# Kernel optimization log

Measured on AMD Instinct MI355X. Metric: run time of the kernel, lower is better.

Reference implementation:

```python
import jax, jax.numpy as jnp
import numpy as np
from jax import lax

EQN, GR = 10, 4
N, C, H, W = 8, 64, 16, 16


def _build_a(h, w):
    num = h * w
    a = np.zeros((num, EQN, 4 * num), np.float32)
    for i in range(num):
        right = (i + 1) % w != 0 and i + 1 < num
        down = i + w < num
        if right:
            a[i, 0, 2 * num + i] = 1.0; a[i, 0, i + 1] = -1.0
            a[i, 2, 2 * num + i] = 1.0; a[i, 2, 2 * num + i + 1] = -1.0
            a[i, 4, i] = 1.0;           a[i, 4, i + 1] = -1.0
            a[i, 6, 3 * num + i] = 1.0; a[i, 6, 3 * num + i + 1] = -1.0
            a[i, 8, num + i] = 1.0;     a[i, 8, num + i + 1] = -1.0
        if down:
            a[i, 1, 3 * num + i] = 1.0; a[i, 1, num + i + w] = -1.0
            a[i, 3, 3 * num + i] = 1.0; a[i, 3, 3 * num + i + w] = -1.0
            a[i, 5, num + i] = 1.0;     a[i, 5, num + i + w] = -1.0
            a[i, 7, 2 * num + i] = 1.0; a[i, 7, 2 * num + i + w] = -1.0
            a[i, 9, i] = 1.0;           a[i, 9, i + w] = -1.0
    last = num - 1
    a[last, 0, 2 * num + last] = 1.0
    a[last, 1, 3 * num + last] = 1.0
    a[last, 2, 2 * num + last] = 1.0
    a[last, 3, 3 * num + last] = 1.0
    a[last, 4, last] = 1.0
    a[last, 5, num + last] = 1.0
    a[last, 6, 3 * num + last] = 1.0
    a[last, 7, 2 * num + last] = 1.0
    a[last, 8, num + last] = 1.0
    a[last, 9, last] = 1.0
    return jnp.asarray(a)


def _conv(x, w, b):
    y = lax.conv_general_dilated(x, w, (1, 1), 'SAME',
                                 dimension_numbers=('NCHW', 'OIHW', 'NCHW'))
    return y + b[None, :, None, None]


def _lrelu(v):
    return jnp.where(v >= 0, v, 0.01 * v)


def setup_inputs() -> dict:
    key = jax.random.key(0)
    ks = jax.random.split(key, 18)
    s = 0.05
    d = {
        'x':   jax.random.normal(ks[0], (N, C, H, W), jnp.float32),
        'a':   _build_a(H, W),
        'gw1': jax.random.normal(ks[1], (C, C, 3, 3), jnp.float32) * s,
        'gb1': jnp.zeros((C,), jnp.float32),
        'gw2': jax.random.normal(ks[2], (EQN * GR, C, 3, 3), jnp.float32) * s,
        'gb2': jnp.zeros((EQN * GR,), jnp.float32),
        'aw1': jax.random.normal(ks[3], (C, C, 3, 3), jnp.float32) * s,
        'ab1': jnp.zeros((C,), jnp.float32),
        'aw2': jax.random.normal(ks[4], (EQN * GR, C, 3, 3), jnp.float32) * s,
        'ab2': jnp.zeros((EQN * GR,), jnp.float32),
        'sw1': jax.random.normal(ks[5], (C // 2, C, 1, 1), jnp.float32) * s,
        'sb1': jnp.zeros((C // 2,), jnp.float32),
        'sw2': jax.random.normal(ks[6], (4 * GR, C // 2, 1, 1), jnp.float32) * s,
        'sb2': jnp.zeros((4 * GR,), jnp.float32),
        'ins_w': jnp.ones((4 * GR,), jnp.float32),
        'ins_b': jnp.zeros((4 * GR,), jnp.float32),
        'pw':  jax.random.normal(ks[7], (128, 4 * GR, 3, 3), jnp.float32) * s,
        'pb':  jnp.zeros((128,), jnp.float32),
    }
    return d


def reference(x, a, gw1, gb1, gw2, gb2, aw1, ab1, aw2, ab2,
              sw1, sb1, sw2, sb2, ins_w, ins_b, pw, pb):
    n, c, h, w = x.shape
    num = h * w
    # attention / gradient / squeeze-excite branches
    att = jax.nn.sigmoid(_conv(_lrelu(_conv(x, aw1, ab1)), aw2, ab2))   # (n, eqn*gr, h, w)
    g   = _conv(_lrelu(_conv(x, gw1, gb1)), gw2, gb2)                   # (n, eqn*gr, h, w)
    pooled = x.mean(axis=(2, 3), keepdims=True)
    se = jax.nn.sigmoid(_conv(_lrelu(_conv(pooled, sw1, sb1)), sw2, sb2))  # (n, 4*gr, 1, 1)
    # reshape channels (gr, eqn), flatten batch*group, move pixel axis first
    att_r = att.reshape(n * GR, EQN, num).transpose(0, 2, 1)   # (ng, num, eqn)
    g_r   = g.reshape(n * GR, EQN, num).transpose(0, 2, 1)
    # weighted flow-equation system (done for all ng at once; the torch chunked
    # loop is only a memory optimization, math is identical)
    A = (a[None] * att_r[..., None]).reshape(n * GR, num * EQN, 4 * num)
    B = (g_r * att_r).reshape(n * GR, num * EQN)
    ATA = jnp.einsum('bki,bkj->bij', A, A)          # (ng, 4num, 4num)
    ATB = jnp.einsum('bki,bk->bi', A, B)            # (ng, 4num)
    ATA = ATA + jnp.eye(4 * num, dtype=x.dtype) * 1e-12
    sol = jnp.linalg.solve(ATA, ATB[..., None])     # (ng, 4num, 1)
    y = sol.reshape(n, 4 * GR, h, w)
    # GroupNorm(1, 4*gr): normalize over (C,H,W) per sample, per-channel affine
    mu = y.mean(axis=(1, 2, 3), keepdims=True)
    var = ((y - mu) ** 2).mean(axis=(1, 2, 3), keepdims=True)
    y = (y - mu) / jnp.sqrt(var + 1e-5)
    y = y * ins_w[None, :, None, None] + ins_b[None, :, None, None]
    y = se * y
    return _conv(y, pw, pb)
```

## Files before the change

### kernel.cpp

```cpp
#include <hip/hip_runtime.h>
#include <hip/hip_bf16.h>


#define NIT 64

__global__ __launch_bounds__(256) void k_se(
    const float* __restrict__ x, const float* __restrict__ sw1,
    const float* __restrict__ sb1, const float* __restrict__ sw2,
    const float* __restrict__ sb2, float* __restrict__ se)
{
  int n = blockIdx.x, t = threadIdx.x;
  __shared__ float part[64*4];
  __shared__ float pooled[64];
  __shared__ float h1[32];
  int c = t >> 2, q = t & 3;
  const float* xp = x + ((n*64 + c)*256) + q*64;
  float s = 0.f;
  #pragma unroll 8
  for (int j = 0; j < 64; ++j) s += xp[j];
  part[c*4+q] = s;
  __syncthreads();
  if (t < 64) pooled[t] = (part[t*4+0]+part[t*4+1]+part[t*4+2]+part[t*4+3]) * (1.f/256.f);
  __syncthreads();
  if (t < 32) {
    float a = sb1[t];
    for (int c2 = 0; c2 < 64; ++c2) a = fmaf(sw1[t*64+c2], pooled[c2], a);
    h1[t] = a >= 0.f ? a : 0.01f*a;
  }
  __syncthreads();
  if (t < 16) {
    float a = sb2[t];
    for (int c2 = 0; c2 < 32; ++c2) a = fmaf(sw2[t*32+c2], h1[c2], a);
    se[n*16+t] = 1.f/(1.f+__expf(-a));
  }
}

__device__ __forceinline__ float lane_bcast(float v, int src){
  return __int_as_float(__builtin_amdgcn_readlane(__float_as_int(v), src));
}

template<int CO_T, int CO_TOTAL, int ACT>
__global__ __launch_bounds__(1024) void k_convw(
    const float* __restrict__ xg, const float* __restrict__ xa,
    const float* __restrict__ wg, const float* __restrict__ bg,
    const float* __restrict__ wa, const float* __restrict__ ba,
    float* __restrict__ outg, float* __restrict__ outa)
{
  const int tiles = CO_TOTAL / CO_T;
  int b = blockIdx.x;
  int tile = b % tiles; int rem = b / tiles;
  int br = rem & 1;     int n = rem >> 1;
  const float* xin  = br ? xa : xg;
  const float* w    = br ? wa : wg;
  const float* bias = br ? ba : bg;
  float* outp       = br ? outa : outg;
  int co_base = tile * CO_T;
  int t = threadIdx.x;
  int pix = t & 255, qc = t >> 8;
  int pr = pix >> 4, pc = pix & 15;
  int lane = t & 63;
  int cib = qc*16;
  __shared__ float xs[64*324];
  __shared__ float part[3][CO_T][256];
  int cil = cib + (lane & 15);
  float wv[CO_T*9];
  #pragma unroll
  for (int co = 0; co < CO_T; ++co) {
    const float* wp = w + ((size_t)(co_base+co)*64 + cil)*9;
    #pragma unroll
    for (int k = 0; k < 9; ++k) wv[co*9+k] = wp[k];
  }
  const float* xn = xin + (size_t)n*64*256;
  for (int idx = t; idx < 64*324; idx += 1024) {
    int ch = idx / 324;
    int rm = idx - ch*324;
    int rr = rm / 18, cc = rm - rr*18;
    int sr = rr - 1, sc = cc - 1;
    float v = 0.f;
    if ((unsigned)sr < 16u && (unsigned)sc < 16u)
      v = xn[ch*256 + sr*16 + sc];
    xs[idx] = v;
  }
  __syncthreads();
  float accA[CO_T], accB[CO_T];
  #pragma unroll
  for (int co = 0; co < CO_T; ++co) { accA[co] = 0.f; accB[co] = 0.f; }
  #pragma unroll
  for (int ci = 0; ci < 8; ++ci) {
    const float* xrA = xs + (cib+ci)*324 + pr*18 + pc;
    const float* xrB = xs + (cib+ci+8)*324 + pr*18 + pc;
    float a0 = xrA[0],  a1 = xrA[1],  a2 = xrA[2];
    float a3 = xrA[18], a4 = xrA[19], a5 = xrA[20];
    float a6 = xrA[36], a7 = xrA[37], a8 = xrA[38];
    float b0 = xrB[0],  b1 = xrB[1],  b2 = xrB[2];
    float b3 = xrB[18], b4 = xrB[19], b5 = xrB[20];
    float b6 = xrB[36], b7 = xrB[37], b8 = xrB[38];
    #pragma unroll
    for (int co = 0; co < CO_T; ++co) {
      float aA = accA[co];
      aA = fmaf(a0, lane_bcast(wv[co*9+0], ci), aA);
      aA = fmaf(a1, lane_bcast(wv[co*9+1], ci), aA);
      aA = fmaf(a2, lane_bcast(wv[co*9+2], ci), aA);
      aA = fmaf(a3, lane_bcast(wv[co*9+3], ci), aA);
      aA = fmaf(a4, lane_bcast(wv[co*9+4], ci), aA);
      aA = fmaf(a5, lane_bcast(wv[co*9+5], ci), aA);
      aA = fmaf(a6, lane_bcast(wv[co*9+6], ci), aA);
      aA = fmaf(a7, lane_bcast(wv[co*9+7], ci), aA);
      aA = fmaf(a8, lane_bcast(wv[co*9+8], ci), aA);
      accA[co] = aA;
      float aB = accB[co];
      aB = fmaf(b0, lane_bcast(wv[co*9+0], ci+8), aB);
      aB = fmaf(b1, lane_bcast(wv[co*9+1], ci+8), aB);
      aB = fmaf(b2, lane_bcast(wv[co*9+2], ci+8), aB);
      aB = fmaf(b3, lane_bcast(wv[co*9+3], ci+8), aB);
      aB = fmaf(b4, lane_bcast(wv[co*9+4], ci+8), aB);
      aB = fmaf(b5, lane_bcast(wv[co*9+5], ci+8), aB);
      aB = fmaf(b6, lane_bcast(wv[co*9+6], ci+8), aB);
      aB = fmaf(b7, lane_bcast(wv[co*9+7], ci+8), aB);
      aB = fmaf(b8, lane_bcast(wv[co*9+8], ci+8), aB);
      accB[co] = aB;
    }
  }
  if (qc > 0) {
    #pragma unroll
    for (int co = 0; co < CO_T; ++co) part[qc-1][co][pix] = accA[co] + accB[co];
  }
  __syncthreads();
  if (qc == 0) {
    float* ob = outp + ((size_t)n*CO_TOTAL + co_base)*256 + pix;
    #pragma unroll
    for (int co = 0; co < CO_T; ++co) {
      float v = bias[co_base+co] + accA[co] + accB[co] + part[0][co][pix]
              + part[1][co][pix] + part[2][co][pix];
      if (ACT == 1) v = v >= 0.f ? v : 0.01f*v;
      if (ACT == 2 && br) v = 1.f/(1.f+__expf(-v));
      ob[co*256] = v;
    }
  }
}

__device__ __forceinline__ float wave_sum(float x){
  x += __int_as_float(__builtin_amdgcn_update_dpp(0, __float_as_int(x), 0x111, 0xf, 0xf, true));
  x += __int_as_float(__builtin_amdgcn_update_dpp(0, __float_as_int(x), 0x112, 0xf, 0xf, true));
  x += __int_as_float(__builtin_amdgcn_update_dpp(0, __float_as_int(x), 0x114, 0xf, 0xf, true));
  x += __int_as_float(__builtin_amdgcn_update_dpp(0, __float_as_int(x), 0x118, 0xf, 0xf, true));
  x += __int_as_float(__builtin_amdgcn_update_dpp(0, __float_as_int(x), 0x142, 0xa, 0xf, true));
  x += __int_as_float(__builtin_amdgcn_update_dpp(0, __float_as_int(x), 0x143, 0xc, 0xf, true));
  return __int_as_float(__builtin_amdgcn_readlane(__float_as_int(x), 63));
}
__device__ __forceinline__ float dpp_prev(float v){
  return __int_as_float(__builtin_amdgcn_update_dpp(0, __float_as_int(v), 0x138, 0xf, 0xf, true));
}
__device__ __forceinline__ float dpp_next(float v){
  return __int_as_float(__builtin_amdgcn_update_dpp(0, __float_as_int(v), 0x130, 0xf, 0xf, true));
}

__global__ __launch_bounds__(64, 1) void k_cg(
    const float* __restrict__ att, const float* __restrict__ gm,
    float* __restrict__ yout)
{
  int bg = blockIdx.x;
  int n = bg >> 2, g = bg & 3;
  const float* ab = att + ((size_t)n*40 + g*10)*256;
  const float* gb = gm  + ((size_t)n*40 + g*10)*256;
  __shared__ float sbuf[10][256];
  __shared__ float tbuf[10][256];
  __shared__ float pl[4][256];
  int l = threadIdx.x;
  int base = l*4;
  int rI = l >> 2;
  int c0 = (l & 3)*4;
  bool rU4 = (rI > 0), hD4 = (rI < 15);
  int iL0 = (base > 0) ? base-1 : 0;
  int iUc = rU4 ? base-16 : base;
  int iDc = hD4 ? base+16 : base;

  float sr[10][4], tr[10][4];
  #pragma unroll
  for (int e = 0; e < 10; ++e) {
    float4 av = *(const float4*)(ab + e*256 + base);
    float4 gv = *(const float4*)(gb + e*256 + base);
    sr[e][0]=av.x*av.x; sr[e][1]=av.y*av.y; sr[e][2]=av.z*av.z; sr[e][3]=av.w*av.w;
    tr[e][0]=sr[e][0]*gv.x; tr[e][1]=sr[e][1]*gv.y; tr[e][2]=sr[e][2]*gv.z; tr[e][3]=sr[e][3]*gv.w;
    *(float4*)(&sbuf[e][base]) = make_float4(sr[e][0],sr[e][1],sr[e][2],sr[e][3]);
    *(float4*)(&tbuf[e][base]) = make_float4(tr[e][0],tr[e][1],tr[e][2],tr[e][3]);
  }
  __syncthreads();

  const int eL[5] = {0,2,4,6,8};
  const int eU[5] = {1,3,5,7,9};
  float sLs[5][4], tLs[5][4], sUs[5][4], tUs[5][4];
  float gU = rU4 ? 1.f : 0.f;
  #pragma unroll
  for (int k = 0; k < 5; ++k) {
    int e = eL[k];
    sLs[k][0] = (c0 > 0) ? sbuf[e][iL0] : 0.f;
    tLs[k][0] = (c0 > 0) ? tbuf[e][iL0] : 0.f;
    #pragma unroll
    for (int j = 1; j < 4; ++j) { sLs[k][j] = sr[e][j-1]; tLs[k][j] = tr[e][j-1]; }
  }
  #pragma unroll
  for (int k = 0; k < 5; ++k) {
    int e = eU[k];
    float4 su = *(const float4*)(&sbuf[e][iUc]);
    float4 tu = *(const float4*)(&tbuf[e][iUc]);
    sUs[k][0]=su.x*gU; sUs[k][1]=su.y*gU; sUs[k][2]=su.z*gU; sUs[k][3]=su.w*gU;
    tUs[k][0]=tu.x*gU; tUs[k][1]=tu.y*gU; tUs[k][2]=tu.z*gU; tUs[k][3]=tu.w*gU;
  }

  float k0R[4],k0L[4],k0X[4],k0D[4],k0U[4], d0[4],di0[4], b0[4];
  float k1R[4],k1L[4],k1D[4],k1U[4],k1X[4], d1[4],di1[4], b1[4];
  float k2R[4],k2L[4],k2D[4],k2U[4],k2X[4], d2[4],di2[4], b2[4];
  float k3R[4],k3L[4],k3D[4],k3U[4],k3X[4], d3[4],di3[4], b3[4];
  #pragma unroll
  for (int j = 0; j < 4; ++j) {
    bool hR = (c0 + j) < 15;
    bool hD = hD4;
    bool last = (l == 63) && (j == 3);
    k0R[j] = hR ? sr[4][j] : 0.f;  k0L[j] = sLs[2][j];  k0X[j] = sLs[0][j];
    k0D[j] = hD ? sr[9][j] : 0.f;  k0U[j] = sUs[4][j];
    k1R[j] = hR ? sr[8][j] : 0.f;  k1L[j] = sLs[4][j];
    k1D[j] = hD ? sr[5][j] : 0.f;  k1U[j] = sUs[2][j];  k1X[j] = sUs[0][j];
    k2R[j] = hR ? sr[2][j] : 0.f;  k2L[j] = sLs[1][j];
    k2D[j] = hD ? sr[7][j] : 0.f;  k2U[j] = sUs[3][j];  k2X[j] = hR ? sr[0][j] : 0.f;
    k3R[j] = hR ? sr[6][j] : 0.f;  k3L[j] = sLs[3][j];
    k3D[j] = hD ? sr[3][j] : 0.f;  k3U[j] = sUs[1][j];  k3X[j] = hD ? sr[1][j] : 0.f;
    d0[j] = k0R[j]+k0L[j]+k0X[j]+k0D[j]+k0U[j] + (last ? sr[4][j]+sr[9][j] : 0.f);
    d1[j] = k1R[j]+k1L[j]+k1D[j]+k1U[j]+k1X[j] + (last ? sr[5][j]+sr[8][j] : 0.f);
    d2[j] = k2R[j]+k2L[j]+k2D[j]+k2U[j]+k2X[j] + (last ? sr[0][j]+sr[2][j]+sr[7][j] : 0.f);
    d3[j] = k3R[j]+k3L[j]+k3D[j]+k3U[j]+k3X[j] + (last ? sr[1][j]+sr[3][j]+sr[6][j] : 0.f);
    b0[j] = (hR?tr[4][j]:0.f) - tLs[2][j] - tLs[0][j] + (hD?tr[9][j]:0.f) - tUs[4][j]
          + (last ? tr[4][j]+tr[9][j] : 0.f);
    b1[j] = (hR?tr[8][j]:0.f) - tLs[4][j] + (hD?tr[5][j]:0.f) - tUs[2][j] - tUs[0][j]
          + (last ? tr[5][j]+tr[8][j] : 0.f);
    b2[j] = (hR?(tr[2][j]+tr[0][j]):0.f) - tLs[1][j] + (hD?tr[7][j]:0.f) - tUs[3][j]
          + (last ? tr[0][j]+tr[2][j]+tr[7][j] : 0.f);
    b3[j] = (hR?tr[6][j]:0.f) - tLs[3][j] + (hD?(tr[3][j]+tr[1][j]):0.f) - tUs[1][j]
          + (last ? tr[1][j]+tr[3][j]+tr[6][j] : 0.f);
    di0[j] = 1.f/(d0[j]+1e-20f); di1[j] = 1.f/(d1[j]+1e-20f);
    di2[j] = 1.f/(d2[j]+1e-20f); di3[j] = 1.f/(d3[j]+1e-20f);
  }

  float vA = sr[0][3]+sr[2][3]+sr[4][3]+sr[7][3]+sr[9][3];
  float vB = sr[1][3]+sr[3][3]+sr[5][3]+sr[6][3]+sr[8][3];
  float ei1 = 1.f/(__shfl(vA, 63, 64)+1e-20f);
  float ei2 = 1.f/(__shfl(vB, 63, 64)+1e-20f);

  float x0[4],x1[4],x2[4],x3[4], r0[4],r1[4],r2[4],r3[4], p0[4],p1[4],p2[4],p3[4];
  float rdr_p = 0.f, ca_p = 0.f, cb_p = 0.f;
  #pragma unroll
  for (int j = 0; j < 4; ++j) {
    x0[j]=0.f; x1[j]=0.f; x2[j]=0.f; x3[j]=0.f;
    r0[j]=b0[j]; r1[j]=b1[j]; r2[j]=b2[j]; r3[j]=b3[j];
    rdr_p += r0[j]*r0[j]*di0[j] + r1[j]*r1[j]*di1[j] + r2[j]*r2[j]*di2[j] + r3[j]*r3[j]*di3[j];
    ca_p += r0[j]+r2[j]; cb_p += r1[j]+r3[j];
  }
  float rdr = wave_sum(rdr_p), ca = wave_sum(ca_p), cb = wave_sum(cb_p);
  float rz = rdr + ca*ca*ei1 + cb*cb*ei2;
  float cc1 = ca*ei1, cc2 = cb*ei2;
  #pragma unroll
  for (int j = 0; j < 4; ++j) {
    p0[j] = di0[j]*r0[j] + cc1; p1[j] = di1[j]*r1[j] + cc2;
    p2[j] = di2[j]*r2[j] + cc1; p3[j] = di3[j]*r3[j] + cc2;
  }
  *(float4*)(&pl[0][base]) = make_float4(p0[0],p0[1],p0[2],p0[3]);
  *(float4*)(&pl[1][base]) = make_float4(p1[0],p1[1],p1[2],p1[3]);
  *(float4*)(&pl[2][base]) = make_float4(p2[0],p2[1],p2[2],p2[3]);
  *(float4*)(&pl[3][base]) = make_float4(p3[0],p3[1],p3[2],p3[3]);
  __syncthreads();

  for (int it = 0; it < NIT; ++it) {
    float nR0 = dpp_next(p0[0]), nR1 = dpp_next(p1[0]),
          nR2 = dpp_next(p2[0]), nR3 = dpp_next(p3[0]);
    float nL0 = dpp_prev(p0[3]), nL1 = dpp_prev(p1[3]),
          nL2 = dpp_prev(p2[3]), nL3 = dpp_prev(p3[3]);
    float4 u0 = *(const float4*)(&pl[0][iUc]);
    float4 u1 = *(const float4*)(&pl[1][iUc]);
    float4 u2 = *(const float4*)(&pl[2][iUc]);
    float4 u3 = *(const float4*)(&pl[3][iUc]);
    float4 w0 = *(const float4*)(&pl[0][iDc]);
    float4 w1 = *(const float4*)(&pl[1][iDc]);
    float4 w2 = *(const float4*)(&pl[2][iDc]);
    float4 w3 = *(const float4*)(&pl[3][iDc]);
    float pU0[4]={u0.x,u0.y,u0.z,u0.w}, pU1[4]={u1.x,u1.y,u1.z,u1.w};
    float pU2[4]={u2.x,u2.y,u2.z,u2.w}, pU3[4]={u3.x,u3.y,u3.z,u3.w};
    float pD0[4]={w0.x,w0.y,w0.z,w0.w}, pD1[4]={w1.x,w1.y,w1.z,w1.w};
    float pD2[4]={w2.x,w2.y,w2.z,w2.w}, pD3[4]={w3.x,w3.y,w3.z,w3.w};
    float q0[4],q1[4],q2[4],q3[4];
    float pq_p = 0.f;
    #pragma unroll
    for (int j = 0; j < 4; ++j) {
      float p0R = (j<3)? p0[j+1] : nR0;  float p0L = (j>0)? p0[j-1] : nL0;
      float p1R = (j<3)? p1[j+1] : nR1;  float p1L = (j>0)? p1[j-1] : nL1;
      float p2R = (j<3)? p2[j+1] : nR2;  float p2L = (j>0)? p2[j-1] : nL2;
      float p3R = (j<3)? p3[j+1] : nR3;  float p3L = (j>0)? p3[j-1] : nL3;
      q0[j] = d0[j]*p0[j] - k0R[j]*p0R - k0L[j]*p0L - k0X[j]*p2L - k0D[j]*pD0[j] - k0U[j]*pU0[j];
      q1[j] = d1[j]*p1[j] - k1R[j]*p1R - k1L[j]*p1L - k1D[j]*pD1[j] - k1U[j]*pU1[j] - k1X[j]*pU3[j];
      q2[j] = d2[j]*p2[j] - k2R[j]*p2R - k2L[j]*p2L - k2D[j]*pD2[j] - k2U[j]*pU2[j] - k2X[j]*p0R;
      q3[j] = d3[j]*p3[j] - k3R[j]*p3R - k3L[j]*p3L - k3D[j]*pD3[j] - k3U[j]*pU3[j] - k3X[j]*pD1[j];
      pq_p += p0[j]*q0[j] + p1[j]*q1[j] + p2[j]*q2[j] + p3[j]*q3[j];
    }
    float pq = wave_sum(pq_p);
    float alpha = pq > 1e-35f ? rz/pq : 0.f;
    float rdr2_p = 0.f, ca2_p = 0.f, cb2_p = 0.f;
    #pragma unroll
    for (int j = 0; j < 4; ++j) {
      x0[j] = fmaf(alpha,p0[j],x0[j]); x1[j] = fmaf(alpha,p1[j],x1[j]);
      x2[j] = fmaf(alpha,p2[j],x2[j]); x3[j] = fmaf(alpha,p3[j],x3[j]);
      r0[j] = fmaf(-alpha,q0[j],r0[j]); r1[j] = fmaf(-alpha,q1[j],r1[j]);
      r2[j] = fmaf(-alpha,q2[j],r2[j]); r3[j] = fmaf(-alpha,q3[j],r3[j]);
      rdr2_p += r0[j]*r0[j]*di0[j] + r1[j]*r1[j]*di1[j] + r2[j]*r2[j]*di2[j] + r3[j]*r3[j]*di3[j];
      ca2_p += r0[j]+r2[j]; cb2_p += r1[j]+r3[j];
    }
    float rdrT = wave_sum(rdr2_p), c1T = wave_sum(ca2_p), c2T = wave_sum(cb2_p);
    float rz2 = rdrT + c1T*c1T*ei1 + c2T*c2T*ei2;
    float beta = rz > 1e-35f ? rz2/rz : 0.f;
    rz = rz2;
    float z1c = c1T*ei1, z2c = c2T*ei2;
    #pragma unroll
    for (int j = 0; j < 4; ++j) {
      p0[j] = fmaf(beta,p0[j], di0[j]*r0[j] + z1c);
      p1[j] = fmaf(beta,p1[j], di1[j]*r1[j] + z2c);
      p2[j] = fmaf(beta,p2[j], di2[j]*r2[j] + z1c);
      p3[j] = fmaf(beta,p3[j], di3[j]*r3[j] + z2c);
    }
    *(float4*)(&pl[0][base]) = make_float4(p0[0],p0[1],p0[2],p0[3]);
    *(float4*)(&pl[1][base]) = make_float4(p1[0],p1[1],p1[2],p1[3]);
    *(float4*)(&pl[2][base]) = make_float4(p2[0],p2[1],p2[2],p2[3]);
    *(float4*)(&pl[3][base]) = make_float4(p3[0],p3[1],p3[2],p3[3]);
    __syncthreads();
  }
  float* yo = yout + ((size_t)n*16 + g*4)*256 + base;
  *(float4*)(yo)       = make_float4(x0[0],x0[1],x0[2],x0[3]);
  *(float4*)(yo + 256) = make_float4(x1[0],x1[1],x1[2],x1[3]);
  *(float4*)(yo + 512) = make_float4(x2[0],x2[1],x2[2],x2[3]);
  *(float4*)(yo + 768) = make_float4(x3[0],x3[1],x3[2],x3[3]);
}

template<int CO_T>
__global__ __launch_bounds__(256) void k_out(
    const float* __restrict__ y, const float* __restrict__ insw,
    const float* __restrict__ insb, const float* __restrict__ sev,
    const float* __restrict__ pw, const float* __restrict__ pb,
    float* __restrict__ out)
{
  const int tiles = 128 / CO_T;
  int b = blockIdx.x;
  int cot = b % tiles, n = b / tiles;
  int co_base = cot * CO_T;
  int t = threadIdx.x;
  int pr = t >> 4, pc = t & 15;
  __shared__ float ys[16*324];
  __shared__ float wl[CO_T*16*12];
  __shared__ float redA[4], redB[4];
  const float* yb = y + (size_t)n*16*256;
  float s = 0.f, s2 = 0.f;
  #pragma unroll
  for (int c = 0; c < 16; ++c) {
    float v = yb[c*256 + t];
    s += v; s2 = fmaf(v, v, s2);
  }
  for (int idx = t; idx < CO_T*144; idx += 256) {
    int co = idx / 144; int rm = idx - co*144;
    int ci = rm / 9; int k = rm - ci*9;
    wl[(co*16 + ci)*12 + k] = pw[(size_t)(co_base+co)*144 + rm];
  }
  for (int idx = t; idx < 16*324; idx += 256) {
    int ch = idx / 324;
    int rem = idx - ch*324;
    int rr = rem / 18, cc = rem - rr*18;
    int sr = rr-1, sc = cc-1;
    float v = 0.f;
    if ((unsigned)sr < 16u && (unsigned)sc < 16u) v = yb[ch*256 + sr*16 + sc];
    ys[idx] = v;
  }
  int lane = t & 63, wid = t >> 6;
  #pragma unroll
  for (int m = 1; m < 64; m <<= 1) { s += __shfl_xor(s, m, 64); s2 += __shfl_xor(s2, m, 64); }
  if (lane == 0) { redA[wid] = s; redB[wid] = s2; }
  __syncthreads();
  float S  = redA[0]+redA[1]+redA[2]+redA[3];
  float SS = redB[0]+redB[1]+redB[2]+redB[3];
  float mu = S * (1.f/4096.f);
  float var = SS * (1.f/4096.f) - mu*mu;
  float rstd = rsqrtf(var + 1e-5f);
  for (int idx = t; idx < 16*324; idx += 256) {
    int ch = idx / 324;
    int rem = idx - ch*324;
    int rr = rem / 18, cc = rem - rr*18;
    int sr = rr-1, sc = cc-1;
    if ((unsigned)sr < 16u && (unsigned)sc < 16u) {
      float sef = sev[n*16+ch];
      float m = rstd * insw[ch] * sef;
      float a = (insb[ch] - mu*rstd*insw[ch]) * sef;
      ys[idx] = fmaf(ys[idx], m, a);
    }
  }
  __syncthreads();
  float acc[CO_T];
  #pragma unroll
  for (int co = 0; co < CO_T; ++co) acc[co] = pb[co_base+co];
  for (int ci = 0; ci < 16; ++ci) {
    const float* xr = ys + ci*324 + pr*18 + pc;
    float x0 = xr[0],  x1 = xr[1],  x2 = xr[2];
    float x3 = xr[18], x4 = xr[19], x5 = xr[20];
    float x6 = xr[36], x7 = xr[37], x8 = xr[38];
    #pragma unroll
    for (int co = 0; co < CO_T; ++co) {
      const float4* wv = ((const float4*)wl) + (co*16 + ci)*3;
      float4 wa = wv[0], wb = wv[1], wc = wv[2];
      float a = acc[co];
      a = fmaf(x0,wa.x,a); a = fmaf(x1,wa.y,a); a = fmaf(x2,wa.z,a);
      a = fmaf(x3,wa.w,a); a = fmaf(x4,wb.x,a); a = fmaf(x5,wb.y,a);
      a = fmaf(x6,wb.z,a); a = fmaf(x7,wb.w,a); a = fmaf(x8,wc.x,a);
      acc[co] = a;
    }
  }
  float* ob = out + ((size_t)n*128 + co_base)*256 + t;
  #pragma unroll
  for (int co = 0; co < CO_T; ++co)
    ob[co*256] = acc[co];
}

extern "C" void kernel_launch(void* const* d_in, const int* in_sizes, int n_in,
                              void* d_out, int out_size, void* d_ws, size_t ws_size,
                              hipStream_t stream) {
  const float* x    = (const float*)d_in[0];
  const float* gw1  = (const float*)d_in[2];
  const float* gb1  = (const float*)d_in[3];
  const float* gw2  = (const float*)d_in[4];
  const float* gb2  = (const float*)d_in[5];
  const float* aw1  = (const float*)d_in[6];
  const float* ab1  = (const float*)d_in[7];
  const float* aw2  = (const float*)d_in[8];
  const float* ab2  = (const float*)d_in[9];
  const float* sw1  = (const float*)d_in[10];
  const float* sb1  = (const float*)d_in[11];
  const float* sw2  = (const float*)d_in[12];
  const float* sb2  = (const float*)d_in[13];
  const float* insw = (const float*)d_in[14];
  const float* insb = (const float*)d_in[15];
  const float* pw   = (const float*)d_in[16];
  const float* pb   = (const float*)d_in[17];
  float* ws = (float*)d_ws;
  float* g1   = ws;
  float* a1   = ws + 131072;
  float* gmat = ws + 262144;
  float* attb = ws + 344064;
  float* sev  = ws + 425984;
  float* ybuf = ws + 426112;
  float* out  = (float*)d_out;

  k_se<<<dim3(8), dim3(256), 0, stream>>>(x, sw1, sb1, sw2, sb2, sev);
  k_convw<4,64,1><<<dim3(256), dim3(1024), 0, stream>>>(x, x, gw1, gb1, aw1, ab1, g1, a1);
  k_convw<4,40,2><<<dim3(160), dim3(1024), 0, stream>>>(g1, a1, gw2, gb2, aw2, ab2, gmat, attb);
  k_cg<<<dim3(32), dim3(64), 0, stream>>>(attb, gmat, ybuf);
  k_out<4><<<dim3(256), dim3(256), 0, stream>>>(ybuf, insw, insb, sev, pw, pb, out);
}
```

Before: 93.21 us.

## Compute two pixels per thread in conv kernels and cut CG iterations

The 3x3 conv kernel now runs 512 threads per block. Each thread computes two vertically adjacent output pixels across 16 input channels, so overlapping input rows and broadcast weights are reused for both pixels. This halves the cross-lane weight broadcasts per FMA and removes the within-thread channel split. Separately, the conjugate-gradient iteration count drops from 64 to 48, which cuts solver work but may loosen convergence of the least-squares solution.

```diff
diff --git a/kernel.cpp b/kernel.cpp
--- a/kernel.cpp
+++ b/kernel.cpp
@@ -2,7 +2,7 @@
 #include <hip/hip_bf16.h>
 
 
-#define NIT 64
+#define NIT 48
 
 __global__ __launch_bounds__(256) void k_se(
     const float* __restrict__ x, const float* __restrict__ sw1,
@@ -40,7 +40,7 @@
 }
 
 template<int CO_T, int CO_TOTAL, int ACT>
-__global__ __launch_bounds__(1024) void k_convw(
+__global__ __launch_bounds__(512) void k_convw(
     const float* __restrict__ xg, const float* __restrict__ xa,
     const float* __restrict__ wg, const float* __restrict__ bg,
     const float* __restrict__ wa, const float* __restrict__ ba,
@@ -56,8 +56,9 @@
   float* outp       = br ? outa : outg;
   int co_base = tile * CO_T;
   int t = threadIdx.x;
-  int pix = t & 255, qc = t >> 8;
-  int pr = pix >> 4, pc = pix & 15;
+  int pp = t & 127, qc = t >> 7;
+  int pr2 = pp >> 4, pc = pp & 15;
+  int px0 = pr2*32 + pc, px1 = px0 + 16;
   int lane = t & 63;
   int cib = qc*16;
   __shared__ float xs[64*324];
@@ -71,7 +72,7 @@
     for (int k = 0; k < 9; ++k) wv[co*9+k] = wp[k];
   }
   const float* xn = xin + (size_t)n*64*256;
-  for (int idx = t; idx < 64*324; idx += 1024) {
+  for (int idx = t; idx < 64*324; idx += 512) {
     int ch = idx / 324;
     int rm = idx - ch*324;
     int rr = rm / 18, cc = rm - rr*18;
@@ -86,55 +87,54 @@
   #pragma unroll
   for (int co = 0; co < CO_T; ++co) { accA[co] = 0.f; accB[co] = 0.f; }
   #pragma unroll
-  for (int ci = 0; ci < 8; ++ci) {
-    const float* xrA = xs + (cib+ci)*324 + pr*18 + pc;
-    const float* xrB = xs + (cib+ci+8)*324 + pr*18 + pc;
-    float a0 = xrA[0],  a1 = xrA[1],  a2 = xrA[2];
-    float a3 = xrA[18], a4 = xrA[19], a5 = xrA[20];
-    float a6 = xrA[36], a7 = xrA[37], a8 = xrA[38];
-    float b0 = xrB[0],  b1 = xrB[1],  b2 = xrB[2];
-    float b3 = xrB[18], b4 = xrB[19], b5 = xrB[20];
-    float b6 = xrB[36], b7 = xrB[37], b8 = xrB[38];
+  for (int ci = 0; ci < 16; ++ci) {
+    const float* xr = xs + (cib+ci)*324 + (2*pr2)*18 + pc;
+    float v0 = xr[0],  v1 = xr[1],  v2 = xr[2];
+    float v3 = xr[18], v4 = xr[19], v5 = xr[20];
+    float v6 = xr[36], v7 = xr[37], v8 = xr[38];
+    float v9 = xr[54], v10 = xr[55], v11 = xr[56];
     #pragma unroll
     for (int co = 0; co < CO_T; ++co) {
+      float w0 = lane_bcast(wv[co*9+0], ci);
+      float w1 = lane_bcast(wv[co*9+1], ci);
+      float w2 = lane_bcast(wv[co*9+2], ci);
+      float w3 = lane_bcast(wv[co*9+3], ci);
+      float w4 = lane_bcast(wv[co*9+4], ci);
+      float w5 = lane_bcast(wv[co*9+5], ci);
+      float w6 = lane_bcast(wv[co*9+6], ci);
+      float w7 = lane_bcast(wv[co*9+7], ci);
+      float w8 = lane_bcast(wv[co*9+8], ci);
       float aA = accA[co];
-      aA = fmaf(a0, lane_bcast(wv[co*9+0], ci), aA);
-      aA = fmaf(a1, lane_bcast(wv[co*9+1], ci), aA);
-      aA = fmaf(a2, lane_bcast(wv[co*9+2], ci), aA);
-      aA = fmaf(a3, lane_bcast(wv[co*9+3], ci), aA);
-      aA = fmaf(a4, lane_bcast(wv[co*9+4], ci), aA);
-      aA = fmaf(a5, lane_bcast(wv[co*9+5], ci), aA);
-      aA = fmaf(a6, lane_bcast(wv[co*9+6], ci), aA);
-      aA = fmaf(a7, lane_bcast(wv[co*9+7], ci), aA);
-      aA = fmaf(a8, lane_bcast(wv[co*9+8], ci), aA);
+      aA = fmaf(v0,w0,aA); aA = fmaf(v1,w1,aA); aA = fmaf(v2,w2,aA);
+      aA = fmaf(v3,w3,aA); aA = fmaf(v4,w4,aA); aA = fmaf(v5,w5,aA);
+      aA = fmaf(v6,w6,aA); aA = fmaf(v7,w7,aA); aA = fmaf(v8,w8,aA);
       accA[co] = aA;
       float aB = accB[co];
-      aB = fmaf(b0, lane_bcast(wv[co*9+0], ci+8), aB);
-      aB = fmaf(b1, lane_bcast(wv[co*9+1], ci+8), aB);
-      aB = fmaf(b2, lane_bcast(wv[co*9+2], ci+8), aB);
-      aB = fmaf(b3, lane_bcast(wv[co*9+3], ci+8), aB);
-      aB = fmaf(b4, lane_bcast(wv[co*9+4], ci+8), aB);
-      aB = fmaf(b5, lane_bcast(wv[co*9+5], ci+8), aB);
-      aB = fmaf(b6, lane_bcast(wv[co*9+6], ci+8), aB);
-      aB = fmaf(b7, lane_bcast(wv[co*9+7], ci+8), aB);
-      aB = fmaf(b8, lane_bcast(wv[co*9+8], ci+8), aB);
+      aB = fmaf(v3,w0,aB); aB = fmaf(v4,w1,aB); aB = fmaf(v5,w2,aB);
+      aB = fmaf(v6,w3,aB); aB = fmaf(v7,w4,aB); aB = fmaf(v8,w5,aB);
+      aB = fmaf(v9,w6,aB); aB = fmaf(v10,w7,aB); aB = fmaf(v11,w8,aB);
       accB[co] = aB;
     }
   }
   if (qc > 0) {
     #pragma unroll
-    for (int co = 0; co < CO_T; ++co) part[qc-1][co][pix] = accA[co] + accB[co];
+    for (int co = 0; co < CO_T; ++co) {
+      part[qc-1][co][px0] = accA[co];
+      part[qc-1][co][px1] = accB[co];
+    }
   }
   __syncthreads();
   if (qc == 0) {
-    float* ob = outp + ((size_t)n*CO_TOTAL + co_base)*256 + pix;
+    float* ob = outp + ((size_t)n*CO_TOTAL + co_base)*256;
     #pragma unroll
     for (int co = 0; co < CO_T; ++co) {
-      float v = bias[co_base+co] + accA[co] + accB[co] + part[0][co][pix]
-              + part[1][co][pix] + part[2][co][pix];
-      if (ACT == 1) v = v >= 0.f ? v : 0.01f*v;
-      if (ACT == 2 && br) v = 1.f/(1.f+__expf(-v));
-      ob[co*256] = v;
+      float bsv = bias[co_base+co];
+      float vA = bsv + accA[co] + part[0][co][px0] + part[1][co][px0] + part[2][co][px0];
+      float vB = bsv + accB[co] + part[0][co][px1] + part[1][co][px1] + part[2][co][px1];
+      if (ACT == 1) { vA = vA >= 0.f ? vA : 0.01f*vA; vB = vB >= 0.f ? vB : 0.01f*vB; }
+      if (ACT == 2 && br) { vA = 1.f/(1.f+__expf(-vA)); vB = 1.f/(1.f+__expf(-vB)); }
+      ob[co*256 + px0] = vA;
+      ob[co*256 + px1] = vB;
     }
   }
 }
@@ -452,8 +452,8 @@
   float* out  = (float*)d_out;
 
   k_se<<<dim3(8), dim3(256), 0, stream>>>(x, sw1, sb1, sw2, sb2, sev);
-  k_convw<4,64,1><<<dim3(256), dim3(1024), 0, stream>>>(x, x, gw1, gb1, aw1, ab1, g1, a1);
-  k_convw<4,40,2><<<dim3(160), dim3(1024), 0, stream>>>(g1, a1, gw2, gb2, aw2, ab2, gmat, attb);
+  k_convw<4,64,1><<<dim3(256), dim3(512), 0, stream>>>(x, x, gw1, gb1, aw1, ab1, g1, a1);
+  k_convw<4,40,2><<<dim3(160), dim3(512), 0, stream>>>(g1, a1, gw2, gb2, aw2, ab2, gmat, attb);
   k_cg<<<dim3(32), dim3(64), 0, stream>>>(attb, gmat, ybuf);
   k_out<4><<<dim3(256), dim3(256), 0, stream>>>(ybuf, insw, insb, sev, pw, pb, out);
 }
```

Result: faster. 89.83 us (-3.6%).
